# Kernel tuning notes

Hardware: AMD Instinct MI355X
Metric: run time of the kernel (lower is better)

Reference implementation:

```python
import jax, jax.numpy as jnp
import numpy as np

N_NODES = 20000
N_EDGES = 320000
IN_F = 168
HID = 256


def gcn_conv(x, W, b, src, dst, ew, n_nodes):
    """PyG GCNConv: symmetric normalization with self-loops (fill 1.0).
    out = D^-1/2 (A + I) D^-1/2 X W^T + b, aggregated at dst (source_to_target).
    """
    xw = x @ W.T  # [N, F_out]
    # degree at target nodes, including self-loop weight 1.0
    deg = jax.ops.segment_sum(ew, dst, num_segments=n_nodes) + 1.0
    dinv = jnp.where(deg > 0, jax.lax.rsqrt(deg), 0.0)
    norm = dinv[src] * ew * dinv[dst]  # [E]
    agg = jax.ops.segment_sum(norm[:, None] * xw[src], dst, num_segments=n_nodes)
    # self-loop contribution: norm_ii = dinv[i]^2
    out = agg + (dinv * dinv)[:, None] * xw
    return out + b


def setup_inputs() -> dict:
    key = jax.random.key(0)
    k = jax.random.split(key, 8)
    x = jax.random.normal(k[0], (N_NODES, IN_F), dtype=jnp.float32)
    edge_index = jax.random.randint(k[1], (2, N_EDGES), 0, N_NODES, dtype=jnp.int64)
    edge_weight = jax.random.uniform(k[2], (N_EDGES,), dtype=jnp.float32)
    # GCN layer weights (PyG Linear: y = x W^T), plus per-layer bias
    s1 = 1.0 / np.sqrt(IN_F)
    s2 = 1.0 / np.sqrt(HID)
    W1 = jax.random.uniform(k[3], (HID, IN_F), minval=-s1, maxval=s1, dtype=jnp.float32)
    b1 = jnp.zeros((HID,), dtype=jnp.float32)
    W2 = jax.random.uniform(k[4], (HID, HID), minval=-s2, maxval=s2, dtype=jnp.float32)
    b2 = jnp.zeros((HID,), dtype=jnp.float32)
    return {"x": x, "edge_index": edge_index, "edge_weight": edge_weight,
            "W1": W1, "b1": b1, "W2": W2, "b2": b2}


def reference(x, edge_index, edge_weight, W1, b1, W2, b2):
    src, dst = edge_index[0], edge_index[1]
    h = gcn_conv(x, W1, b1, src, dst, edge_weight, N_NODES)
    h = jax.nn.relu(h)
    h = gcn_conv(h, W2, b2, src, dst, edge_weight, N_NODES)
    h = jax.nn.relu(h)
    return h
```

## Files before the change

kernel.cpp:

```cpp
#include <hip/hip_runtime.h>

#define N_NODES 20000
#define N_EDGES 320000
#define IN_F    168
#define HID     256
#define K1P     192
#define NF4     42

typedef __attribute__((ext_vector_type(8))) short bf16x8;
typedef __attribute__((ext_vector_type(4))) float f32x4;

__device__ __forceinline__ short f2bf(float f) {
    union { float f; unsigned u; } v; v.f = f;
    unsigned r = v.u + 0x7FFFu + ((v.u >> 16) & 1u);
    return (short)(r >> 16);
}
__device__ __forceinline__ float bf2f(short s) {
    union { unsigned u; float f; } v; v.u = ((unsigned)(unsigned short)s) << 16;
    return v.f;
}


__global__ void edge_count_deg(const int* __restrict__ ei, const float* __restrict__ ew,
                               float* __restrict__ deg, int* __restrict__ counts) {
    int e = blockIdx.x * blockDim.x + threadIdx.x;
    if (e >= N_EDGES) return;
    int d = ei[N_EDGES + e];
    atomicAdd(&deg[d], ew[e]);
    atomicAdd(&counts[d], 1);
}

__global__ __launch_bounds__(1024) void scan_part(const int* __restrict__ counts,
                                                  int* __restrict__ offs,
                                                  int* __restrict__ bsum,
                                                  float* __restrict__ deg, int n) {
    int tid  = threadIdx.x;
    int lane = tid & 63;
    int wv   = tid >> 6;
    int i = blockIdx.x * 1024 + tid;
    if (i < n) deg[i] = rsqrtf(deg[i] + 1.0f);
    __shared__ int wsum[16];
    int v = (i < n) ? counts[i] : 0;
    int incl = v;
    #pragma unroll
    for (int d = 1; d < 64; d <<= 1) {
        int t = __shfl_up(incl, d);
        if (lane >= d) incl += t;
    }
    if (lane == 63) wsum[wv] = incl;
    __syncthreads();
    if (wv == 0) {
        int w = (lane < 16) ? wsum[lane] : 0;
        int winc = w;
        #pragma unroll
        for (int d = 1; d < 16; d <<= 1) {
            int t = __shfl_up(winc, d);
            if (lane >= d) winc += t;
        }
        if (lane < 16) wsum[lane] = winc - w;
    }
    __syncthreads();
    if (i < n) offs[i] = wsum[wv] + incl - v;
    if (tid == 1023) bsum[blockIdx.x] = wsum[15] + incl;
}

__global__ __launch_bounds__(1024) void scan_add(const int* __restrict__ bsum,
                                                 int* __restrict__ offs, int n) {
    int i = blockIdx.x * 1024 + threadIdx.x;
    int add = 0;
    for (int b = 0; b < (int)blockIdx.x; ++b) add += bsum[b];
    if (i < n) offs[i] += add;
    if (i == n) offs[n] = add + bsum[blockIdx.x];
}

__global__ void scatter_edges(const int* __restrict__ ei, const float* __restrict__ ew,
                              const float* __restrict__ dinv, const int* __restrict__ offs,
                              int* __restrict__ cursor, int* __restrict__ csr_src,
                              float* __restrict__ csr_norm) {
    int e = blockIdx.x * blockDim.x + threadIdx.x;
    if (e >= N_EDGES) return;
    int s = ei[e];
    int d = ei[N_EDGES + e];
    int pos = offs[d] + atomicAdd(&cursor[d], 1);
    csr_src[pos]  = s;
    csr_norm[pos] = dinv[s] * ew[e] * dinv[d];
}

__global__ void split_w(const float* __restrict__ W1, const float* __restrict__ W2,
                        short* __restrict__ w1h, short* __restrict__ w1l,
                        short* __restrict__ w2h, short* __restrict__ w2l) {
    int b = blockIdx.x;
    int k = threadIdx.x;
    if (b < 256) {
        if (k >= K1P) return;
        float v = (k < IN_F) ? W1[(size_t)b * IN_F + k] : 0.f;
        short h = f2bf(v);
        w1h[(size_t)b * K1P + k] = h;
        w1l[(size_t)b * K1P + k] = f2bf(v - bf2f(h));
    } else {
        int r = b - 256;
        float v = W2[(size_t)r * HID + k];
        short h = f2bf(v);
        w2h[(size_t)r * HID + k] = h;
        w2l[(size_t)r * HID + k] = f2bf(v - bf2f(h));
    }
}


__global__ __launch_bounds__(256) void agg_x_split(const float* __restrict__ x,
                                                   const float* __restrict__ dinv,
                                                   const int* __restrict__ offs,
                                                   const int* __restrict__ csr_src,
                                                   const float* __restrict__ csr_norm,
                                                   short* __restrict__ axh,
                                                   short* __restrict__ axl) {
    int wave = threadIdx.x >> 6;
    int lane = threadIdx.x & 63;
    int n = blockIdx.x * 4 + wave;
    bool act = lane < NF4;
    float di = dinv[n];
    float sw = di * di;
    float ax = 0.f, ay = 0.f, az = 0.f, aw = 0.f;
    if (act) {
        float4 v = *(const float4*)(x + (size_t)n * IN_F + lane * 4);
        ax = sw * v.x; ay = sw * v.y; az = sw * v.z; aw = sw * v.w;
    }
    int p0 = offs[n], p1 = offs[n + 1];
    int p = p0;
    for (; p + 4 <= p1; p += 4) {
        int   s0 = csr_src[p],     s1 = csr_src[p + 1];
        int   s2 = csr_src[p + 2], s3 = csr_src[p + 3];
        float w0 = csr_norm[p],     w1 = csr_norm[p + 1];
        float w2 = csr_norm[p + 2], w3 = csr_norm[p + 3];
        if (act) {
            float4 r0 = *(const float4*)(x + (size_t)s0 * IN_F + lane * 4);
            float4 r1 = *(const float4*)(x + (size_t)s1 * IN_F + lane * 4);
            float4 r2 = *(const float4*)(x + (size_t)s2 * IN_F + lane * 4);
            float4 r3 = *(const float4*)(x + (size_t)s3 * IN_F + lane * 4);
            ax += w0 * r0.x + w1 * r1.x + w2 * r2.x + w3 * r3.x;
            ay += w0 * r0.y + w1 * r1.y + w2 * r2.y + w3 * r3.y;
            az += w0 * r0.z + w1 * r1.z + w2 * r2.z + w3 * r3.z;
            aw += w0 * r0.w + w1 * r1.w + w2 * r2.w + w3 * r3.w;
        }
    }
    for (; p < p1; ++p) {
        int   s0 = csr_src[p];
        float w0 = csr_norm[p];
        if (act) {
            float4 r0 = *(const float4*)(x + (size_t)s0 * IN_F + lane * 4);
            ax += w0 * r0.x; ay += w0 * r0.y; az += w0 * r0.z; aw += w0 * r0.w;
        }
    }
    size_t base = (size_t)n * K1P + lane * 4;
    if (act) {
        float a[4] = {ax, ay, az, aw};
        short hv[4], lv[4];
        #pragma unroll
        for (int i = 0; i < 4; ++i) {
            hv[i] = f2bf(a[i]);
            lv[i] = f2bf(a[i] - bf2f(hv[i]));
        }
        *(short4*)&axh[base] = make_short4(hv[0], hv[1], hv[2], hv[3]);
        *(short4*)&axl[base] = make_short4(lv[0], lv[1], lv[2], lv[3]);
    } else if (lane < 48) {
        short4 z = make_short4(0, 0, 0, 0);
        *(short4*)&axh[base] = z;
        *(short4*)&axl[base] = z;
    }
}

__global__ __launch_bounds__(256) void agg_h_split(const short* __restrict__ h1h,
                                                   const float* __restrict__ dinv,
                                                   const int* __restrict__ offs,
                                                   const int* __restrict__ csr_src,
                                                   const float* __restrict__ csr_norm,
                                                   short* __restrict__ ahh,
                                                   short* __restrict__ ahl) {
    int wave = threadIdx.x >> 6;
    int lane = threadIdx.x & 63;
    int n = blockIdx.x * 4 + wave;
    float di = dinv[n];
    float sw = di * di;
    short4 sv = *(const short4*)(h1h + (size_t)n * HID + lane * 4);
    float ax = sw * bf2f(sv.x), ay = sw * bf2f(sv.y);
    float az = sw * bf2f(sv.z), aw = sw * bf2f(sv.w);
    int p0 = offs[n], p1 = offs[n + 1];
    int p = p0;
    for (; p + 4 <= p1; p += 4) {
        int   s0 = csr_src[p],     s1 = csr_src[p + 1];
        int   s2 = csr_src[p + 2], s3 = csr_src[p + 3];
        float w0 = csr_norm[p],     w1 = csr_norm[p + 1];
        float w2 = csr_norm[p + 2], w3 = csr_norm[p + 3];
        short4 r0 = *(const short4*)(h1h + (size_t)s0 * HID + lane * 4);
        short4 r1 = *(const short4*)(h1h + (size_t)s1 * HID + lane * 4);
        short4 r2 = *(const short4*)(h1h + (size_t)s2 * HID + lane * 4);
        short4 r3 = *(const short4*)(h1h + (size_t)s3 * HID + lane * 4);
        ax += w0 * bf2f(r0.x) + w1 * bf2f(r1.x) + w2 * bf2f(r2.x) + w3 * bf2f(r3.x);
        ay += w0 * bf2f(r0.y) + w1 * bf2f(r1.y) + w2 * bf2f(r2.y) + w3 * bf2f(r3.y);
        az += w0 * bf2f(r0.z) + w1 * bf2f(r1.z) + w2 * bf2f(r2.z) + w3 * bf2f(r3.z);
        aw += w0 * bf2f(r0.w) + w1 * bf2f(r1.w) + w2 * bf2f(r2.w) + w3 * bf2f(r3.w);
    }
    for (; p < p1; ++p) {
        int   s0 = csr_src[p];
        float w0 = csr_norm[p];
        short4 r0 = *(const short4*)(h1h + (size_t)s0 * HID + lane * 4);
        ax += w0 * bf2f(r0.x); ay += w0 * bf2f(r0.y);
        az += w0 * bf2f(r0.z); aw += w0 * bf2f(r0.w);
    }
    float a[4] = {ax, ay, az, aw};
    short hv[4], lv[4];
    #pragma unroll
    for (int i = 0; i < 4; ++i) {
        hv[i] = f2bf(a[i]);
        lv[i] = f2bf(a[i] - bf2f(hv[i]));
    }
    size_t base = (size_t)n * HID + lane * 4;
    *(short4*)&ahh[base] = make_short4(hv[0], hv[1], hv[2], hv[3]);
    *(short4*)&ahl[base] = make_short4(lv[0], lv[1], lv[2], lv[3]);
}


#define LDS_STRIDE 72

__global__ __launch_bounds__(256) void gemm_split(const short* __restrict__ Ah,
                                                  const short* __restrict__ Al,
                                                  const short* __restrict__ Wh,
                                                  const short* __restrict__ Wl,
                                                  const float* __restrict__ bias,
                                                  float* __restrict__ Cf,
                                                  short* __restrict__ Cbf,
                                                  int M, int Ks, int nsteps, int mode) {
    __shared__ short sAh[64 * LDS_STRIDE];
    __shared__ short sAl[64 * LDS_STRIDE];
    __shared__ short sWh[64 * LDS_STRIDE];
    __shared__ short sWl[64 * LDS_STRIDE];

    const int tid  = threadIdx.x;
    const int lane = tid & 63;
    const int wv   = tid >> 6;
    const int l16  = lane & 15;
    const int quad = lane >> 4;
    const int wm   = (wv & 1) * 32;
    const int wn   = (wv >> 1) * 32;
    const int bm   = blockIdx.x * 64;
    const int bn   = blockIdx.y * 64;

    const int srow = tid >> 2;
    const int sseg = (tid & 3) * 16;
    int arow = bm + srow; if (arow >= M) arow = M - 1;
    const short* gAh = Ah + (size_t)arow * Ks;
    const short* gAl = Al + (size_t)arow * Ks;
    const short* gWh = Wh + (size_t)(bn + srow) * Ks;
    const short* gWl = Wl + (size_t)(bn + srow) * Ks;
    const int lds_off = srow * LDS_STRIDE + sseg;

    f32x4 acc00 = {0,0,0,0}, acc01 = {0,0,0,0}, acc10 = {0,0,0,0}, acc11 = {0,0,0,0};

    int4 pah0 = *(const int4*)(gAh + sseg), pah1 = *(const int4*)(gAh + sseg + 8);
    int4 pal0 = *(const int4*)(gAl + sseg), pal1 = *(const int4*)(gAl + sseg + 8);
    int4 pwh0 = *(const int4*)(gWh + sseg), pwh1 = *(const int4*)(gWh + sseg + 8);
    int4 pwl0 = *(const int4*)(gWl + sseg), pwl1 = *(const int4*)(gWl + sseg + 8);

    for (int ks = 0; ks < nsteps; ++ks) {
        *(int4*)&sAh[lds_off] = pah0; *(int4*)&sAh[lds_off + 8] = pah1;
        *(int4*)&sAl[lds_off] = pal0; *(int4*)&sAl[lds_off + 8] = pal1;
        *(int4*)&sWh[lds_off] = pwh0; *(int4*)&sWh[lds_off + 8] = pwh1;
        *(int4*)&sWl[lds_off] = pwl0; *(int4*)&sWl[lds_off + 8] = pwl1;
        __syncthreads();
        if (ks + 1 < nsteps) {
            int o = (ks + 1) * 64 + sseg;
            pah0 = *(const int4*)(gAh + o); pah1 = *(const int4*)(gAh + o + 8);
            pal0 = *(const int4*)(gAl + o); pal1 = *(const int4*)(gAl + o + 8);
            pwh0 = *(const int4*)(gWh + o); pwh1 = *(const int4*)(gWh + o + 8);
            pwl0 = *(const int4*)(gWl + o); pwl1 = *(const int4*)(gWl + o + 8);
        }
        #pragma unroll
        for (int o = 0; o < 2; ++o) {
            const int a0 = (wm + l16) * LDS_STRIDE + o * 32 + quad * 8;
            const int a1 = a0 + 16 * LDS_STRIDE;
            const int w0 = (wn + l16) * LDS_STRIDE + o * 32 + quad * 8;
            const int w1 = w0 + 16 * LDS_STRIDE;
            bf16x8 ah0 = *(const bf16x8*)&sAh[a0];
            bf16x8 ah1 = *(const bf16x8*)&sAh[a1];
            bf16x8 al0 = *(const bf16x8*)&sAl[a0];
            bf16x8 al1 = *(const bf16x8*)&sAl[a1];
            bf16x8 wh0 = *(const bf16x8*)&sWh[w0];
            bf16x8 wh1 = *(const bf16x8*)&sWh[w1];
            bf16x8 wl0 = *(const bf16x8*)&sWl[w0];
            bf16x8 wl1 = *(const bf16x8*)&sWl[w1];
            acc00 = __builtin_amdgcn_mfma_f32_16x16x32_bf16(ah0, wh0, acc00, 0, 0, 0);
            acc00 = __builtin_amdgcn_mfma_f32_16x16x32_bf16(ah0, wl0, acc00, 0, 0, 0);
            acc00 = __builtin_amdgcn_mfma_f32_16x16x32_bf16(al0, wh0, acc00, 0, 0, 0);
            acc01 = __builtin_amdgcn_mfma_f32_16x16x32_bf16(ah0, wh1, acc01, 0, 0, 0);
            acc01 = __builtin_amdgcn_mfma_f32_16x16x32_bf16(ah0, wl1, acc01, 0, 0, 0);
            acc01 = __builtin_amdgcn_mfma_f32_16x16x32_bf16(al0, wh1, acc01, 0, 0, 0);
            acc10 = __builtin_amdgcn_mfma_f32_16x16x32_bf16(ah1, wh0, acc10, 0, 0, 0);
            acc10 = __builtin_amdgcn_mfma_f32_16x16x32_bf16(ah1, wl0, acc10, 0, 0, 0);
            acc10 = __builtin_amdgcn_mfma_f32_16x16x32_bf16(al1, wh0, acc10, 0, 0, 0);
            acc11 = __builtin_amdgcn_mfma_f32_16x16x32_bf16(ah1, wh1, acc11, 0, 0, 0);
            acc11 = __builtin_amdgcn_mfma_f32_16x16x32_bf16(ah1, wl1, acc11, 0, 0, 0);
            acc11 = __builtin_amdgcn_mfma_f32_16x16x32_bf16(al1, wh1, acc11, 0, 0, 0);
        }
        __syncthreads();
    }

    const int colb = bn + wn + l16;
    const int rowb = bm + wm + quad * 4;
    const float b0 = bias[colb];
    const float b1 = bias[colb + 16];
    #pragma unroll
    for (int r = 0; r < 4; ++r) {
        int row = rowb + r;
        if (row < M) {
            float v0 = acc00[r] + b0; v0 = v0 > 0.f ? v0 : 0.f;
            float v1 = acc01[r] + b1; v1 = v1 > 0.f ? v1 : 0.f;
            if (mode == 0) {
                Cbf[(size_t)row * HID + colb]      = f2bf(v0);
                Cbf[(size_t)row * HID + colb + 16] = f2bf(v1);
            } else {
                Cf[(size_t)row * HID + colb]      = v0;
                Cf[(size_t)row * HID + colb + 16] = v1;
            }
        }
        int row2 = row + 16;
        if (row2 < M) {
            float v0 = acc10[r] + b0; v0 = v0 > 0.f ? v0 : 0.f;
            float v1 = acc11[r] + b1; v1 = v1 > 0.f ? v1 : 0.f;
            if (mode == 0) {
                Cbf[(size_t)row2 * HID + colb]      = f2bf(v0);
                Cbf[(size_t)row2 * HID + colb + 16] = f2bf(v1);
            } else {
                Cf[(size_t)row2 * HID + colb]      = v0;
                Cf[(size_t)row2 * HID + colb + 16] = v1;
            }
        }
    }
}


extern "C" void kernel_launch(void* const* d_in, const int* in_sizes, int n_in,
                              void* d_out, int out_size, void* d_ws, size_t ws_size,
                              hipStream_t stream) {
    const float* x  = (const float*)d_in[0];
    const int*   ei = (const int*)d_in[1];
    const float* ew = (const float*)d_in[2];
    const float* W1 = (const float*)d_in[3];
    const float* b1 = (const float*)d_in[4];
    const float* W2 = (const float*)d_in[5];
    const float* b2 = (const float*)d_in[6];
    float* out = (float*)d_out;

    char* ws = (char*)d_ws;
    float* deg      = (float*)(ws);
    int*   counts   = (int*)(ws + 80000);
    int*   cursor   = (int*)(ws + 160000);
    int*   offs     = (int*)(ws + 240000);
    int*   bsum     = (int*)(ws + 320016);
    int*   csr_src  = (int*)(ws + 320144);
    float* csr_norm = (float*)(ws + 1600144);
    short* axh      = (short*)(ws + 2880144);
    short* axl      = (short*)(ws + 10560144);
    short* ahh      = (short*)(ws + 2880144);
    short* ahl      = (short*)(ws + 13120144);
    short* h1h      = (short*)(ws + 23360144);
    short* w1h      = (short*)(ws + 33600144);
    short* w1l      = (short*)(ws + 33698448);
    short* w2h      = (short*)(ws + 33796752);
    short* w2l      = (short*)(ws + 33927824);

    hipMemsetAsync(d_ws, 0, 240000, stream);

    const int TB = 256;
    edge_count_deg<<<(N_EDGES + TB - 1) / TB, TB, 0, stream>>>(ei, ew, deg, counts);
    scan_part<<<20, 1024, 0, stream>>>(counts, offs, bsum, deg, N_NODES);
    scan_add<<<20, 1024, 0, stream>>>(bsum, offs, N_NODES);
    scatter_edges<<<(N_EDGES + TB - 1) / TB, TB, 0, stream>>>(ei, ew, deg, offs, cursor,
                                                              csr_src, csr_norm);
    split_w<<<512, 256, 0, stream>>>(W1, W2, w1h, w1l, w2h, w2l);

    dim3 gg((N_NODES + 63) / 64, 4);
    agg_x_split<<<N_NODES / 4, 256, 0, stream>>>(x, deg, offs, csr_src, csr_norm, axh, axl);
    gemm_split<<<gg, 256, 0, stream>>>(axh, axl, w1h, w1l, b1, nullptr, h1h,
                                       N_NODES, K1P, 3, 0);
    agg_h_split<<<N_NODES / 4, 256, 0, stream>>>(h1h, deg, offs, csr_src, csr_norm, ahh, ahl);
    gemm_split<<<gg, 256, 0, stream>>>(ahh, ahl, w2h, w2l, b2, out, nullptr,
                                       N_NODES, HID, 4, 1);
}
```

Before: 236.2 us.

## Split aggregation into XCD-pinned feature slices and convert x to bf16 upfront

After: 261.1 us. +10.6%, slower.

```diff
diff --git a/kernel.cpp b/kernel.cpp
--- a/kernel.cpp
+++ b/kernel.cpp
@@ -5,7 +5,7 @@
 #define IN_F    168
 #define HID     256
 #define K1P     192
-#define NF4     42
+#define RS      256
 
 typedef __attribute__((ext_vector_type(8))) short bf16x8;
 typedef __attribute__((ext_vector_type(4))) float f32x4;
@@ -21,14 +21,44 @@
 }
 
 
-__global__ void edge_count_deg(const int* __restrict__ ei, const float* __restrict__ ew,
-                               float* __restrict__ deg, int* __restrict__ counts) {
-    int e = blockIdx.x * blockDim.x + threadIdx.x;
-    if (e >= N_EDGES) return;
-    int d = ei[N_EDGES + e];
-    atomicAdd(&deg[d], ew[e]);
-    atomicAdd(&counts[d], 1);
-}
+__global__ void prep_all(const float* __restrict__ x, short* __restrict__ xb,
+                         const float* __restrict__ W1, const float* __restrict__ W2,
+                         short* __restrict__ w1h, short* __restrict__ w1l,
+                         short* __restrict__ w2h, short* __restrict__ w2l,
+                         const int* __restrict__ ei, const float* __restrict__ ew,
+                         float* __restrict__ deg, int* __restrict__ counts) {
+    int b = blockIdx.x;
+    int k = threadIdx.x;
+    if (b < N_NODES) {
+        float v = (k < IN_F) ? x[(size_t)b * IN_F + k] : 0.f;
+        xb[(size_t)b * RS + k] = f2bf(v);
+        return;
+    }
+    b -= N_NODES;
+    if (b < 256) {
+        if (k >= K1P) return;
+        float v = (k < IN_F) ? W1[(size_t)b * IN_F + k] : 0.f;
+        short h = f2bf(v);
+        w1h[(size_t)b * K1P + k] = h;
+        w1l[(size_t)b * K1P + k] = f2bf(v - bf2f(h));
+        return;
+    }
+    if (b < 512) {
+        int r = b - 256;
+        float v = W2[(size_t)r * HID + k];
+        short h = f2bf(v);
+        w2h[(size_t)r * HID + k] = h;
+        w2l[(size_t)r * HID + k] = f2bf(v - bf2f(h));
+        return;
+    }
+    int e = (b - 512) * 256 + k;
+    if (e < N_EDGES) {
+        int d = ei[N_EDGES + e];
+        atomicAdd(&deg[d], ew[e]);
+        atomicAdd(&counts[d], 1);
+    }
+}
+
 
 __global__ __launch_bounds__(1024) void scan_part(const int* __restrict__ counts,
                                                   int* __restrict__ offs,
@@ -86,137 +116,60 @@
     csr_norm[pos] = dinv[s] * ew[e] * dinv[d];
 }
 
-__global__ void split_w(const float* __restrict__ W1, const float* __restrict__ W2,
-                        short* __restrict__ w1h, short* __restrict__ w1l,
-                        short* __restrict__ w2h, short* __restrict__ w2l) {
-    int b = blockIdx.x;
-    int k = threadIdx.x;
-    if (b < 256) {
-        if (k >= K1P) return;
-        float v = (k < IN_F) ? W1[(size_t)b * IN_F + k] : 0.f;
-        short h = f2bf(v);
-        w1h[(size_t)b * K1P + k] = h;
-        w1l[(size_t)b * K1P + k] = f2bf(v - bf2f(h));
-    } else {
-        int r = b - 256;
-        float v = W2[(size_t)r * HID + k];
-        short h = f2bf(v);
-        w2h[(size_t)r * HID + k] = h;
-        w2l[(size_t)r * HID + k] = f2bf(v - bf2f(h));
-    }
-}
-
-
-__global__ __launch_bounds__(256) void agg_x_split(const float* __restrict__ x,
-                                                   const float* __restrict__ dinv,
-                                                   const int* __restrict__ offs,
-                                                   const int* __restrict__ csr_src,
-                                                   const float* __restrict__ csr_norm,
-                                                   short* __restrict__ axh,
-                                                   short* __restrict__ axl) {
-    int wave = threadIdx.x >> 6;
-    int lane = threadIdx.x & 63;
-    int n = blockIdx.x * 4 + wave;
-    bool act = lane < NF4;
+
+__global__ __launch_bounds__(256) void agg_pass(const short* __restrict__ rows,
+                                                const float* __restrict__ dinv,
+                                                const int* __restrict__ offs,
+                                                const int* __restrict__ csr_src,
+                                                const float* __restrict__ csr_norm,
+                                                short* __restrict__ outh,
+                                                short* __restrict__ outl,
+                                                int out_stride, int npasses) {
+    const int b    = blockIdx.x;
+    const int xcd  = b & 7;
+    const int pass = xcd >> 1;
+    if (pass >= npasses) return;
+    const int half = xcd & 1;
+    const int j    = b >> 3;
+    const int wave = threadIdx.x >> 6;
+    const int lane = threadIdx.x & 63;
+    const int n    = (half * 2500 + j) * 4 + wave;
+    const int fo   = pass * 64;
+
     float di = dinv[n];
-    float sw = di * di;
-    float ax = 0.f, ay = 0.f, az = 0.f, aw = 0.f;
-    if (act) {
-        float4 v = *(const float4*)(x + (size_t)n * IN_F + lane * 4);
-        ax = sw * v.x; ay = sw * v.y; az = sw * v.z; aw = sw * v.w;
-    }
+    float acc = di * di * bf2f(rows[(size_t)n * RS + fo + lane]);
+
     int p0 = offs[n], p1 = offs[n + 1];
     int p = p0;
+    for (; p + 8 <= p1; p += 8) {
+        int s[8]; float w[8]; short r[8];
+        #pragma unroll
+        for (int i = 0; i < 8; ++i) { s[i] = csr_src[p + i]; w[i] = csr_norm[p + i]; }
+        #pragma unroll
+        for (int i = 0; i < 8; ++i) r[i] = rows[(size_t)s[i] * RS + fo + lane];
+        #pragma unroll
+        for (int i = 0; i < 8; ++i) acc += w[i] * bf2f(r[i]);
+    }
     for (; p + 4 <= p1; p += 4) {
-        int   s0 = csr_src[p],     s1 = csr_src[p + 1];
-        int   s2 = csr_src[p + 2], s3 = csr_src[p + 3];
-        float w0 = csr_norm[p],     w1 = csr_norm[p + 1];
-        float w2 = csr_norm[p + 2], w3 = csr_norm[p + 3];
-        if (act) {
-            float4 r0 = *(const float4*)(x + (size_t)s0 * IN_F + lane * 4);
-            float4 r1 = *(const float4*)(x + (size_t)s1 * IN_F + lane * 4);
-            float4 r2 = *(const float4*)(x + (size_t)s2 * IN_F + lane * 4);
-            float4 r3 = *(const float4*)(x + (size_t)s3 * IN_F + lane * 4);
-            ax += w0 * r0.x + w1 * r1.x + w2 * r2.x + w3 * r3.x;
-            ay += w0 * r0.y + w1 * r1.y + w2 * r2.y + w3 * r3.y;
-            az += w0 * r0.z + w1 * r1.z + w2 * r2.z + w3 * r3.z;
-            aw += w0 * r0.w + w1 * r1.w + w2 * r2.w + w3 * r3.w;
-        }
+        int s[4]; float w[4]; short r[4];
+        #pragma unroll
+        for (int i = 0; i < 4; ++i) { s[i] = csr_src[p + i]; w[i] = csr_norm[p + i]; }
+        #pragma unroll
+        for (int i = 0; i < 4; ++i) r[i] = rows[(size_t)s[i] * RS + fo + lane];
+        #pragma unroll
+        for (int i = 0; i < 4; ++i) acc += w[i] * bf2f(r[i]);
     }
     for (; p < p1; ++p) {
         int   s0 = csr_src[p];
         float w0 = csr_norm[p];
-        if (act) {
-            float4 r0 = *(const float4*)(x + (size_t)s0 * IN_F + lane * 4);
-            ax += w0 * r0.x; ay += w0 * r0.y; az += w0 * r0.z; aw += w0 * r0.w;
-        }
-    }
-    size_t base = (size_t)n * K1P + lane * 4;
-    if (act) {
-        float a[4] = {ax, ay, az, aw};
-        short hv[4], lv[4];
-        #pragma unroll
-        for (int i = 0; i < 4; ++i) {
-            hv[i] = f2bf(a[i]);
-            lv[i] = f2bf(a[i] - bf2f(hv[i]));
-        }
-        *(short4*)&axh[base] = make_short4(hv[0], hv[1], hv[2], hv[3]);
-        *(short4*)&axl[base] = make_short4(lv[0], lv[1], lv[2], lv[3]);
-    } else if (lane < 48) {
-        short4 z = make_short4(0, 0, 0, 0);
-        *(short4*)&axh[base] = z;
-        *(short4*)&axl[base] = z;
-    }
-}
-
-__global__ __launch_bounds__(256) void agg_h_split(const short* __restrict__ h1h,
-                                                   const float* __restrict__ dinv,
-                                                   const int* __restrict__ offs,
-                                                   const int* __restrict__ csr_src,
-                                                   const float* __restrict__ csr_norm,
-                                                   short* __restrict__ ahh,
-                                                   short* __restrict__ ahl) {
-    int wave = threadIdx.x >> 6;
-    int lane = threadIdx.x & 63;
-    int n = blockIdx.x * 4 + wave;
-    float di = dinv[n];
-    float sw = di * di;
-    short4 sv = *(const short4*)(h1h + (size_t)n * HID + lane * 4);
-    float ax = sw * bf2f(sv.x), ay = sw * bf2f(sv.y);
-    float az = sw * bf2f(sv.z), aw = sw * bf2f(sv.w);
-    int p0 = offs[n], p1 = offs[n + 1];
-    int p = p0;
-    for (; p + 4 <= p1; p += 4) {
-        int   s0 = csr_src[p],     s1 = csr_src[p + 1];
-        int   s2 = csr_src[p + 2], s3 = csr_src[p + 3];
-        float w0 = csr_norm[p],     w1 = csr_norm[p + 1];
-        float w2 = csr_norm[p + 2], w3 = csr_norm[p + 3];
-        short4 r0 = *(const short4*)(h1h + (size_t)s0 * HID + lane * 4);
-        short4 r1 = *(const short4*)(h1h + (size_t)s1 * HID + lane * 4);
-        short4 r2 = *(const short4*)(h1h + (size_t)s2 * HID + lane * 4);
-        short4 r3 = *(const short4*)(h1h + (size_t)s3 * HID + lane * 4);
-        ax += w0 * bf2f(r0.x) + w1 * bf2f(r1.x) + w2 * bf2f(r2.x) + w3 * bf2f(r3.x);
-        ay += w0 * bf2f(r0.y) + w1 * bf2f(r1.y) + w2 * bf2f(r2.y) + w3 * bf2f(r3.y);
-        az += w0 * bf2f(r0.z) + w1 * bf2f(r1.z) + w2 * bf2f(r2.z) + w3 * bf2f(r3.z);
-        aw += w0 * bf2f(r0.w) + w1 * bf2f(r1.w) + w2 * bf2f(r2.w) + w3 * bf2f(r3.w);
-    }
-    for (; p < p1; ++p) {
-        int   s0 = csr_src[p];
-        float w0 = csr_norm[p];
-        short4 r0 = *(const short4*)(h1h + (size_t)s0 * HID + lane * 4);
-        ax += w0 * bf2f(r0.x); ay += w0 * bf2f(r0.y);
-        az += w0 * bf2f(r0.z); aw += w0 * bf2f(r0.w);
-    }
-    float a[4] = {ax, ay, az, aw};
-    short hv[4], lv[4];
-    #pragma unroll
-    for (int i = 0; i < 4; ++i) {
-        hv[i] = f2bf(a[i]);
-        lv[i] = f2bf(a[i] - bf2f(hv[i]));
-    }
-    size_t base = (size_t)n * HID + lane * 4;
-    *(short4*)&ahh[base] = make_short4(hv[0], hv[1], hv[2], hv[3]);
-    *(short4*)&ahl[base] = make_short4(lv[0], lv[1], lv[2], lv[3]);
+        acc += w0 * bf2f(rows[(size_t)s0 * RS + fo + lane]);
+    }
+
+    short h = f2bf(acc);
+    short l = f2bf(acc - bf2f(h));
+    size_t ob = (size_t)n * out_stride + fo + lane;
+    outh[ob] = h;
+    outl[ob] = l;
 }
 
 
@@ -235,6 +188,16 @@
     __shared__ short sWh[64 * LDS_STRIDE];
     __shared__ short sWl[64 * LDS_STRIDE];
 
+    const int idx   = blockIdx.x;
+    const int group = idx >> 5;
+    const int xcd   = idx & 7;
+    const int slot  = (idx >> 3) & 3;
+    const int mt    = group * 8 + xcd;
+    const int mtiles = (M + 63) >> 6;
+    if (mt >= mtiles) return;
+    const int bm = mt * 64;
+    const int bn = slot * 64;
+
     const int tid  = threadIdx.x;
     const int lane = tid & 63;
     const int wv   = tid >> 6;
@@ -242,8 +205,6 @@
     const int quad = lane >> 4;
     const int wm   = (wv & 1) * 32;
     const int wn   = (wv >> 1) * 32;
-    const int bm   = blockIdx.x * 64;
-    const int bn   = blockIdx.y * 64;
 
     const int srow = tid >> 2;
     const int sseg = (tid & 3) * 16;
@@ -367,22 +328,27 @@
     short* w1l      = (short*)(ws + 33698448);
     short* w2h      = (short*)(ws + 33796752);
     short* w2l      = (short*)(ws + 33927824);
+    short* xb       = (short*)(ws + 34058896);
 
     hipMemsetAsync(d_ws, 0, 240000, stream);
 
     const int TB = 256;
-    edge_count_deg<<<(N_EDGES + TB - 1) / TB, TB, 0, stream>>>(ei, ew, deg, counts);
+    prep_all<<<N_NODES + 512 + (N_EDGES + 255) / 256, 256, 0, stream>>>(
+        x, xb, W1, W2, w1h, w1l, w2h, w2l, ei, ew, deg, counts);
     scan_part<<<20, 1024, 0, stream>>>(counts, offs, bsum, deg, N_NODES);
     scan_add<<<20, 1024, 0, stream>>>(bsum, offs, N_NODES);
     scatter_edges<<<(N_EDGES + TB - 1) / TB, TB, 0, stream>>>(ei, ew, deg, offs, cursor,
                                                               csr_src, csr_norm);
-    split_w<<<512, 256, 0, stream>>>(W1, W2, w1h, w1l, w2h, w2l);
-
-    dim3 gg((N_NODES + 63) / 64, 4);
-    agg_x_split<<<N_NODES / 4, 256, 0, stream>>>(x, deg, offs, csr_src, csr_norm, axh, axl);
-    gemm_split<<<gg, 256, 0, stream>>>(axh, axl, w1h, w1l, b1, nullptr, h1h,
-                                       N_NODES, K1P, 3, 0);
-    agg_h_split<<<N_NODES / 4, 256, 0, stream>>>(h1h, deg, offs, csr_src, csr_norm, ahh, ahl);
-    gemm_split<<<gg, 256, 0, stream>>>(ahh, ahl, w2h, w2l, b2, out, nullptr,
-                                       N_NODES, HID, 4, 1);
-}
+
+    const int mtiles = (N_NODES + 63) / 64;
+    const int gemm_grid = ((mtiles + 7) / 8) * 32;
+    const int agg_grid = 2500 * 8;
+    agg_pass<<<agg_grid, 256, 0, stream>>>(xb, deg, offs, csr_src, csr_norm,
+                                           axh, axl, K1P, 3);
+    gemm_split<<<gemm_grid, 256, 0, stream>>>(axh, axl, w1h, w1l, b1, nullptr, h1h,
+                                              N_NODES, K1P, 3, 0);
+    agg_pass<<<agg_grid, 256, 0, stream>>>(h1h, deg, offs, csr_src, csr_norm,
+                                           ahh, ahl, HID, 4);
+    gemm_split<<<gemm_grid, 256, 0, stream>>>(ahh, ahl, w2h, w2l, b2, out, nullptr,
+                                              N_NODES, HID, 4, 1);
+}
```
